# Kernel optimization log

Hardware: AMD Instinct MI355X
Metric: run time of the kernel (lower is better)

The kernel has to match this reference:

```python
import jax, jax.numpy as jnp
import numpy as np
import math

HIDDEN = 128; NHEADS = 4; N_COE = 50; N_SCALES = 4; THRE = 5.0; S = 4096; B = 1


def setup_inputs():
    key = jax.random.key(0)
    ks = jax.random.split(key, 12)
    w = lambda k, shape: jax.random.normal(k, shape, jnp.float32) * 0.05
    return {
        "eigenvalue": jax.random.uniform(ks[0], (B, S), jnp.float32) * 2.0,  # graph Laplacian eigvals in [0,2)
        "length": jnp.full((B,), S, dtype=jnp.int32),
        "sele_num": jnp.full((B,), S, dtype=jnp.int32),
        "eig_w_W": w(ks[1], (HIDDEN + 1, HIDDEN)), "eig_w_b": jnp.zeros((HIDDEN,), jnp.float32),
        "mha_ln_g": jnp.ones((HIDDEN,), jnp.float32), "mha_ln_b": jnp.zeros((HIDDEN,), jnp.float32),
        "in_W": w(ks[2], (HIDDEN, 3 * HIDDEN)), "in_b": jnp.zeros((3 * HIDDEN,), jnp.float32),
        "out_W": w(ks[3], (HIDDEN, HIDDEN)), "out_b": jnp.zeros((HIDDEN,), jnp.float32),
        "ffn_ln_g": jnp.ones((HIDDEN,), jnp.float32), "ffn_ln_b": jnp.zeros((HIDDEN,), jnp.float32),
        "ffn1_W": w(ks[4], (HIDDEN, HIDDEN)), "ffn1_b": jnp.zeros((HIDDEN,), jnp.float32),
        "ffn2_W": w(ks[5], (HIDDEN, HIDDEN)), "ffn2_b": jnp.zeros((HIDDEN,), jnp.float32),
        "dsc_W": w(ks[6], (HIDDEN, N_COE)), "dsc_b": jnp.zeros((N_COE,), jnp.float32),
        "dwv_W": w(ks[7], (HIDDEN, N_COE)), "dwv_b": jnp.zeros((N_COE,), jnp.float32),
        "dss_W": w(ks[8], (HIDDEN, N_SCALES)), "dss_b": jnp.zeros((N_SCALES,), jnp.float32),
    }


def layer_norm(x, g, b, eps=1e-5):
    m = x.mean(-1, keepdims=True)
    v = ((x - m) ** 2).mean(-1, keepdims=True)
    return (x - m) / jnp.sqrt(v + eps) * g + b


def sine_encoding(e, W, b):
    # e: [B, S] -> [B, S, HIDDEN]
    div = jnp.exp(jnp.arange(0, HIDDEN, 2, dtype=e.dtype) * (-math.log(10000.0) / HIDDEN))
    pe = (e * 100.0)[..., None] * div  # [B, S, HIDDEN/2]
    eeig = jnp.concatenate([e[..., None], jnp.sin(pe), jnp.cos(pe)], axis=-1)  # [B, S, HIDDEN+1]
    return eeig @ W + b


def mha(x, pad_mask, in_W, in_b, out_W, out_b):
    # x: [B, S, D]; pad_mask: [B, S] True = masked key
    Bb, Ss, D = x.shape
    hd = D // NHEADS
    qkv = x @ in_W + in_b
    q, k, v = jnp.split(qkv, 3, axis=-1)
    hsplit = lambda t: t.reshape(Bb, Ss, NHEADS, hd).transpose(0, 2, 1, 3)  # [B, H, S, hd]
    q, k, v = hsplit(q), hsplit(k), hsplit(v)
    scores = jnp.einsum('bhqd,bhkd->bhqk', q, k) / math.sqrt(hd)
    scores = jnp.where(pad_mask[:, None, None, :], -jnp.inf, scores)
    attn = jax.nn.softmax(scores, axis=-1)
    o = jnp.einsum('bhqk,bhkd->bhqd', attn, v).transpose(0, 2, 1, 3).reshape(Bb, Ss, D)
    return o @ out_W + out_b


def cheb_base(y, n_coe, flag):
    # Chebyshev recurrence: wavelet = [T_0, T_2, ...], scaling = [T_1, T_3, ...]
    te0 = jnp.ones_like(y)
    to0 = y
    def step(carry, _):
        te, to = carry
        te = 2.0 * y * to - te
        to = 2.0 * y * te - to
        return (te, to), (te, to)
    _, (evens, odds) = jax.lax.scan(step, (te0, to0), None, length=n_coe - 1)
    if flag == 'scaling':
        base = jnp.concatenate([to0[None], odds], axis=0)   # [n_coe, B, S, d]
    else:
        base = jnp.concatenate([te0[None], evens], axis=0)
    return jnp.moveaxis(base, 0, 1)  # [B, n_coe, S, d]


def _forward(eigenvalue, eig_w_W, eig_w_b, mha_ln_g, mha_ln_b, in_W, in_b, out_W, out_b,
             ffn_ln_g, ffn_ln_b, ffn1_W, ffn1_b, ffn2_W, ffn2_b,
             dsc_W, dsc_b, dwv_W, dwv_b, dss_W, dss_b, length, sele_num):
    Bb, Ss = eigenvalue.shape
    eve = eigenvalue
    eig_mask = jnp.arange(Ss)[None, :] >= sele_num[:, None]  # [B, S] True = pad
    # --- EigenEncoding (dropout in eval mode = identity) ---
    eig = sine_encoding(eve, eig_w_W, eig_w_b)
    eig = eig + mha(layer_norm(eig, mha_ln_g, mha_ln_b), eig_mask, in_W, in_b, out_W, out_b)
    f = layer_norm(eig, ffn_ln_g, ffn_ln_b)
    f = jax.nn.gelu(f @ ffn1_W + ffn1_b, approximate=False) @ ffn2_W + ffn2_b
    eig_filter = eig + f  # [B, S, HIDDEN]
    lenf = length.astype(eve.dtype)[:, None]
    def pooled(W, b):
        c = eig_filter @ W + b
        c = jnp.where(eig_mask[..., None], 0.0, c)
        return c.sum(axis=1) / (lenf + 1e-8)
    coe_scaling = jax.nn.sigmoid(pooled(dsc_W, dsc_b))
    coe_scaling = coe_scaling / (coe_scaling.sum(-1, keepdims=True) + 1e-8)  # [B, n_coe]
    coe_wavelet = jax.nn.sigmoid(pooled(dwv_W, dwv_b))
    coe_wavelet = coe_wavelet / (coe_wavelet.sum(-1, keepdims=True) + 1e-8)
    coe_scales = jax.nn.sigmoid(pooled(dss_W, dss_b)) * THRE  # [B, n_scales]
    # --- Chebyshev bases ---
    base_scaling = cheb_base(eve[..., None] - 1.0, N_COE, 'scaling')  # [B, n_coe, S, 1]
    fsw = eve[..., None] * coe_scales[:, None, :]                      # [B, S, n_scales]
    fsw = jnp.where(fsw > 2.0, 0.0, fsw)
    base_wavelet = cheb_base(fsw - 1.0, N_COE, 'wavelet')             # [B, n_coe, S, n_scales]
    base_scaling = 0.5 * (1.0 - base_scaling)
    base_wavelet = 0.5 * (1.0 - base_wavelet)
    curr_scaling = jnp.einsum('bc,bcsd->bsd', coe_scaling, base_scaling)
    curr_wavelet = jnp.einsum('bc,bcsd->bsd', coe_wavelet, base_wavelet)
    out = jnp.concatenate([curr_scaling, curr_wavelet], axis=-1)       # [B, S, 1+n_scales]
    out = out / (jnp.linalg.norm(out, axis=-1, keepdims=True) + 1e-8)  # cfg.lam.tight_use = True
    return out


def reference(eigenvalue, length, sele_num, eig_w_W, eig_w_b, mha_ln_g, mha_ln_b, in_W, in_b,
              out_W, out_b, ffn_ln_g, ffn_ln_b, ffn1_W, ffn1_b, ffn2_W, ffn2_b,
              dsc_W, dsc_b, dwv_W, dwv_b, dss_W, dss_b):
    return _forward(eigenvalue, eig_w_W, eig_w_b, mha_ln_g, mha_ln_b, in_W, in_b, out_W, out_b,
                    ffn_ln_g, ffn_ln_b, ffn1_W, ffn1_b, ffn2_W, ffn2_b,
                    dsc_W, dsc_b, dwv_W, dwv_b, dss_W, dss_b, length, sele_num)
```

## Files before the change

kernel.cpp:

```cpp
#include <hip/hip_runtime.h>
#include <math.h>


#define KSPLIT 4

typedef __attribute__((ext_vector_type(8))) short short8;
typedef __attribute__((ext_vector_type(4))) short short4v;
typedef __attribute__((ext_vector_type(4))) float f32x4;

__device__ inline unsigned short f2bf(float x) {
    unsigned u = __float_as_uint(x);
    return (unsigned short)((u + 0x7FFFu + ((u >> 16) & 1u)) >> 16);
}
__device__ inline float bf2f(unsigned short h) { return __uint_as_float(((unsigned)h) << 16); }

__global__ __launch_bounds__(512) void k_embed(const float* __restrict__ eve,
    const float* __restrict__ eigW, const float* __restrict__ ebias,
    const float* __restrict__ g, const float* __restrict__ b,
    const float* __restrict__ inW, const float* __restrict__ inb,
    float* __restrict__ eig, float* __restrict__ qkv, unsigned short* __restrict__ Khi_g,
    unsigned short* __restrict__ Klo_g, unsigned short* __restrict__ Vt_g,
    float* __restrict__ xsum)
{
    __shared__ __align__(16) float wsh[129 * 128];
    __shared__ __align__(16) float se[16][132];
    __shared__ __align__(16) float xn[16][132];
    __shared__ __align__(16) unsigned short vsh[16][136];
    const int t = threadIdx.x;
    const int r0 = blockIdx.x * 16;
    if (blockIdx.x == 0 && t < 128) xsum[t] = 0.f;
    {
        const int r = t >> 5, l5 = t & 31;
        const float e = eve[r0 + r];
        if (l5 == 0) se[r][128] = e;
        #pragma unroll
        for (int jj = 0; jj < 2; ++jj) {
            const int j = l5 * 2 + jj;
            const float div = __expf(-0.07195578415606394f * (float)(2 * j));
            const float pe = e * 100.0f * div;
            se[r][j]      = __sinf(pe);
            se[r][64 + j] = __cosf(pe);
        }
    }
    {
        const float4* __restrict__ src = (const float4*)eigW;
        float4* dst = (float4*)wsh;
        #pragma unroll
        for (int i = 0; i < 9; ++i) {
            const int f = t + i * 512;
            if (f < 4128) dst[f] = src[f];
        }
    }
    __syncthreads();
    const int r  = t >> 5;
    const int c0 = (t & 31) * 4;
    float xa[4];
    {
        const float4 w0 = *(const float4*)&wsh[c0];
        const float ea = se[r][128];
        float a0 = ea * w0.x, a1 = ea * w0.y, a2 = ea * w0.z, a3 = ea * w0.w;
        #pragma unroll 8
        for (int k = 0; k < 128; ++k) {
            const float xv = se[r][k];
            const float4 wk = *(const float4*)&wsh[(k + 1) * 128 + c0];
            a0 = fmaf(xv, wk.x, a0); a1 = fmaf(xv, wk.y, a1);
            a2 = fmaf(xv, wk.z, a2); a3 = fmaf(xv, wk.w, a3);
        }
        const float4 bb = *(const float4*)&ebias[c0];
        xa[0] = a0 + bb.x; xa[1] = a1 + bb.y; xa[2] = a2 + bb.z; xa[3] = a3 + bb.w;
        *(float4*)&eig[(size_t)(r0 + r) * 128 + c0] = make_float4(xa[0], xa[1], xa[2], xa[3]);
    }
    {
        float sa = (xa[0] + xa[1]) + (xa[2] + xa[3]);
        float qa = (xa[0] * xa[0] + xa[1] * xa[1]) + (xa[2] * xa[2] + xa[3] * xa[3]);
        #pragma unroll
        for (int m = 1; m < 32; m <<= 1) {
            sa += __shfl_xor(sa, m, 32); qa += __shfl_xor(qa, m, 32);
        }
        const float ma = sa * (1.f / 128.f);
        const float ia = 1.f / sqrtf(qa * (1.f / 128.f) - ma * ma + 1e-5f);
        const float4 gg = *(const float4*)&g[c0];
        const float4 bb = *(const float4*)&b[c0];
        *(float4*)&xn[r][c0] = make_float4((xa[0] - ma) * ia * gg.x + bb.x,
                                           (xa[1] - ma) * ia * gg.y + bb.y,
                                           (xa[2] - ma) * ia * gg.z + bb.z,
                                           (xa[3] - ma) * ia * gg.w + bb.w);
    }
    const int row = r0 + r;
    for (int p = 0; p < 3; ++p) {
        __syncthreads();
        {
            const float4* __restrict__ src = (const float4*)inW;
            float4* dst = (float4*)wsh;
            #pragma unroll
            for (int i = 0; i < 8; ++i) {
                const int f = t + i * 512;
                const int k = f >> 5, c4 = f & 31;
                dst[f] = src[k * 96 + p * 32 + c4];
            }
        }
        __syncthreads();
        float A[4];
        {
            const float4 bb = *(const float4*)&inb[p * 128 + c0];
            A[0] = bb.x; A[1] = bb.y; A[2] = bb.z; A[3] = bb.w;
        }
        #pragma unroll 8
        for (int k = 0; k < 128; ++k) {
            const float xv = xn[r][k];
            const float4 wk = *(const float4*)&wsh[k * 128 + c0];
            A[0] = fmaf(xv, wk.x, A[0]); A[1] = fmaf(xv, wk.y, A[1]);
            A[2] = fmaf(xv, wk.z, A[2]); A[3] = fmaf(xv, wk.w, A[3]);
        }
        if (p == 0) {
            *(float4*)&qkv[(size_t)row * 384 + c0] = make_float4(A[0], A[1], A[2], A[3]);
        } else if (p == 1) {
            const int h = c0 >> 5, d = c0 & 31;
            unsigned short h4[4], l4v[4];
            #pragma unroll
            for (int i = 0; i < 4; ++i) { h4[i] = f2bf(A[i]); l4v[i] = f2bf(A[i] - bf2f(h4[i])); }
            *(uint2*)&Khi_g[((size_t)h * 4096 + row) * 32 + d] = *(uint2*)h4;
            *(uint2*)&Klo_g[((size_t)h * 4096 + row) * 32 + d] = *(uint2*)l4v;
        } else {
            unsigned short v4[4];
            #pragma unroll
            for (int i = 0; i < 4; ++i) v4[i] = f2bf(A[i]);
            *(uint2*)&vsh[r][c0] = *(uint2*)v4;
        }
    }
    __syncthreads();
    if (t < 128) {
        unsigned short tmp[16];
        #pragma unroll
        for (int k2 = 0; k2 < 16; ++k2) tmp[k2] = vsh[k2][t];
        *(uint4*)&Vt_g[(size_t)t * 4096 + r0]     = *(uint4*)&tmp[0];
        *(uint4*)&Vt_g[(size_t)t * 4096 + r0 + 8] = *(uint4*)&tmp[8];
    }
}

#define KSTR 40
#define VSTR 72
#define PSTR 72

__global__ __launch_bounds__(256) void k_attn(const float* __restrict__ qkv,
    const unsigned short* __restrict__ Khi_g, const unsigned short* __restrict__ Klo_g,
    const unsigned short* __restrict__ Vt_g,
    const int* __restrict__ sele, float* __restrict__ Oe, float* __restrict__ E)
{
    __shared__ __align__(16) unsigned short Khi[64 * KSTR];
    __shared__ __align__(16) unsigned short Klo[64 * KSTR];
    __shared__ __align__(16) unsigned short Vt[32 * VSTR];
    __shared__ __align__(16) unsigned short Pb[4][16 * PSTR];

    const int t = threadIdx.x;
    const int lane = t & 63;
    const int l = lane & 15;
    const int quad = lane >> 4;
    const int wv = __builtin_amdgcn_readfirstlane(t >> 6);
    const int qb = blockIdx.x;
    const int h  = blockIdx.y;
    const int ks = blockIdx.z;
    const int nk = sele[0];

    short8 qhi, qlo;
    {
        const float* __restrict__ qr = qkv + (size_t)(qb * 64 + wv * 16 + l) * 384 + h * 32 + quad * 8;
        const float4 a = *(const float4*)qr;
        const float4 b = *(const float4*)(qr + 4);
        const float sc = 0.17677669529663687f;
        float v[8] = {a.x * sc, a.y * sc, a.z * sc, a.w * sc, b.x * sc, b.y * sc, b.z * sc, b.w * sc};
        #pragma unroll
        for (int j = 0; j < 8; ++j) {
            const unsigned short hb = f2bf(v[j]);
            qhi[j] = (short)hb;
            qlo[j] = (short)f2bf(v[j] - bf2f(hb));
        }
    }
    f32x4 accO0 = {0.f, 0.f, 0.f, 0.f};
    f32x4 accO1 = {0.f, 0.f, 0.f, 0.f};
    float elane = 0.f;

    const int kk = t >> 2;
    const int d0 = (t & 3) * 8;
    const int vd = t >> 3;
    const int ko = (t & 7) * 8;

    for (int ch = 0; ch < 16; ++ch) {
        const int keybase = ks * 1024 + ch * 64;
        __syncthreads();
        {
            const uint4 kh16 = *(const uint4*)&Khi_g[((size_t)h * 4096 + keybase + kk) * 32 + d0];
            const uint4 kl16 = *(const uint4*)&Klo_g[((size_t)h * 4096 + keybase + kk) * 32 + d0];
            const uint4 vv16 = *(const uint4*)&Vt_g[((size_t)h * 32 + vd) * 4096 + keybase + ko];
            *(uint4*)&Khi[kk * KSTR + d0] = kh16;
            *(uint4*)&Klo[kk * KSTR + d0] = kl16;
            *(uint4*)&Vt[vd * VSTR + ko]  = vv16;
        }
        __syncthreads();
        unsigned short* __restrict__ Pw = Pb[wv];
        #pragma unroll
        for (int tile = 0; tile < 4; ++tile) {
            const int kl = tile * 16 + l;
            const short8 kh = *(const short8*)&Khi[kl * KSTR + quad * 8];
            const short8 kw = *(const short8*)&Klo[kl * KSTR + quad * 8];
            f32x4 S = {0.f, 0.f, 0.f, 0.f};
            S = __builtin_amdgcn_mfma_f32_16x16x32_bf16(kh, qhi, S, 0, 0, 0);
            S = __builtin_amdgcn_mfma_f32_16x16x32_bf16(kw, qhi, S, 0, 0, 0);
            S = __builtin_amdgcn_mfma_f32_16x16x32_bf16(kh, qlo, S, 0, 0, 0);
            const int kg0 = keybase + tile * 16 + quad * 4;
            short4v pw;
            #pragma unroll
            for (int r = 0; r < 4; ++r) {
                const float p = (kg0 + r < nk) ? __expf(S[r]) : 0.f;
                elane += p;
                pw[r] = (short)f2bf(p);
            }
            *(short4v*)&Pw[l * PSTR + tile * 16 + quad * 4] = pw;
        }
        #pragma unroll
        for (int step = 0; step < 2; ++step) {
            const short8 pa  = *(const short8*)&Pw[l * PSTR + step * 32 + quad * 8];
            const short8 vb0 = *(const short8*)&Vt[l * VSTR + step * 32 + quad * 8];
            const short8 vb1 = *(const short8*)&Vt[(16 + l) * VSTR + step * 32 + quad * 8];
            accO0 = __builtin_amdgcn_mfma_f32_16x16x32_bf16(pa, vb0, accO0, 0, 0, 0);
            accO1 = __builtin_amdgcn_mfma_f32_16x16x32_bf16(pa, vb1, accO1, 0, 0, 0);
        }
    }
    elane += __shfl_xor(elane, 16, 64);
    elane += __shfl_xor(elane, 32, 64);
    const int qrow0 = qb * 64 + wv * 16;
    if (lane < 16)
        E[((size_t)ks * 4 + h) * 4096 + qrow0 + l] = elane;
    #pragma unroll
    for (int r = 0; r < 4; ++r) {
        const size_t row = qrow0 + quad * 4 + r;
        Oe[((size_t)ks * 4096 + row) * 128 + h * 32 + l]      = accO0[r];
        Oe[((size_t)ks * 4096 + row) * 128 + h * 32 + 16 + l] = accO1[r];
    }
}

__global__ __launch_bounds__(512) void k_ffn(const float* __restrict__ eig,
    const float* __restrict__ Oe, const float* __restrict__ E,
    const float* __restrict__ outW, const float* __restrict__ outb,
    const float* __restrict__ lg, const float* __restrict__ lb,
    const float* __restrict__ W1, const float* __restrict__ b1,
    const float* __restrict__ W2, const float* __restrict__ b2,
    const int* __restrict__ sele, float* __restrict__ xsum)
{
    __shared__ __align__(16) float wsh[128 * 128];
    __shared__ __align__(16) float sA[16][132];
    __shared__ __align__(16) float xn[16][132];
    __shared__ __align__(16) float cs[16][132];
    const int t = threadIdx.x;
    const int r0 = blockIdx.x * 16;
    const int r  = t >> 5;
    const int c0 = (t & 31) * 4;
    {
        const int h = c0 >> 5;
        float es = 0.f;
        float v[4] = {0.f, 0.f, 0.f, 0.f};
        #pragma unroll
        for (int ks = 0; ks < KSPLIT; ++ks) {
            es += E[((size_t)ks * 4 + h) * 4096 + r0 + r];
            const float4 o1 = *(const float4*)&Oe[((size_t)ks * 4096 + r0 + r) * 128 + c0];
            v[0] += o1.x; v[1] += o1.y; v[2] += o1.z; v[3] += o1.w;
        }
        const float rcp = 1.f / es;
        *(float4*)&sA[r][c0] = make_float4(v[0] * rcp, v[1] * rcp, v[2] * rcp, v[3] * rcp);
    }
    {
        const float4* __restrict__ src = (const float4*)outW;
        float4* dst = (float4*)wsh;
        #pragma unroll
        for (int i = 0; i < 8; ++i) dst[t + i * 512] = src[t + i * 512];
    }
    __syncthreads();
    float x2[4];
    {
        const float4 bb = *(const float4*)&outb[c0];
        float a0 = bb.x, a1 = bb.y, a2 = bb.z, a3 = bb.w;
        #pragma unroll 8
        for (int k = 0; k < 128; ++k) {
            const float xv = sA[r][k];
            const float4 wk = *(const float4*)&wsh[k * 128 + c0];
            a0 = fmaf(xv, wk.x, a0); a1 = fmaf(xv, wk.y, a1);
            a2 = fmaf(xv, wk.z, a2); a3 = fmaf(xv, wk.w, a3);
        }
        const float4 ea = *(const float4*)&eig[(size_t)(r0 + r) * 128 + c0];
        x2[0] = ea.x + a0; x2[1] = ea.y + a1; x2[2] = ea.z + a2; x2[3] = ea.w + a3;
    }
    {
        float sa = (x2[0] + x2[1]) + (x2[2] + x2[3]);
        float qa = (x2[0] * x2[0] + x2[1] * x2[1]) + (x2[2] * x2[2] + x2[3] * x2[3]);
        #pragma unroll
        for (int m = 1; m < 32; m <<= 1) {
            sa += __shfl_xor(sa, m, 32); qa += __shfl_xor(qa, m, 32);
        }
        const float ma = sa * (1.f / 128.f);
        const float ia = 1.f / sqrtf(qa * (1.f / 128.f) - ma * ma + 1e-5f);
        const float4 gg = *(const float4*)&lg[c0];
        const float4 bb = *(const float4*)&lb[c0];
        *(float4*)&xn[r][c0] = make_float4((x2[0] - ma) * ia * gg.x + bb.x,
                                           (x2[1] - ma) * ia * gg.y + bb.y,
                                           (x2[2] - ma) * ia * gg.z + bb.z,
                                           (x2[3] - ma) * ia * gg.w + bb.w);
    }
    __syncthreads();
    {
        const float4* __restrict__ src = (const float4*)W1;
        float4* dst = (float4*)wsh;
        #pragma unroll
        for (int i = 0; i < 8; ++i) dst[t + i * 512] = src[t + i * 512];
    }
    __syncthreads();
    {
        const float4 bb = *(const float4*)&b1[c0];
        float a0 = bb.x, a1 = bb.y, a2 = bb.z, a3 = bb.w;
        #pragma unroll 8
        for (int k = 0; k < 128; ++k) {
            const float xv = xn[r][k];
            const float4 wk = *(const float4*)&wsh[k * 128 + c0];
            a0 = fmaf(xv, wk.x, a0); a1 = fmaf(xv, wk.y, a1);
            a2 = fmaf(xv, wk.z, a2); a3 = fmaf(xv, wk.w, a3);
        }
        *(float4*)&sA[r][c0] = make_float4(
            0.5f * a0 * (1.f + erff(a0 * 0.70710678118654752f)),
            0.5f * a1 * (1.f + erff(a1 * 0.70710678118654752f)),
            0.5f * a2 * (1.f + erff(a2 * 0.70710678118654752f)),
            0.5f * a3 * (1.f + erff(a3 * 0.70710678118654752f)));
    }
    __syncthreads();
    {
        const float4* __restrict__ src = (const float4*)W2;
        float4* dst = (float4*)wsh;
        #pragma unroll
        for (int i = 0; i < 8; ++i) dst[t + i * 512] = src[t + i * 512];
    }
    __syncthreads();
    {
        const float4 bb = *(const float4*)&b2[c0];
        float a0 = bb.x, a1 = bb.y, a2 = bb.z, a3 = bb.w;
        #pragma unroll 8
        for (int k = 0; k < 128; ++k) {
            const float xv = sA[r][k];
            const float4 wk = *(const float4*)&wsh[k * 128 + c0];
            a0 = fmaf(xv, wk.x, a0); a1 = fmaf(xv, wk.y, a1);
            a2 = fmaf(xv, wk.z, a2); a3 = fmaf(xv, wk.w, a3);
        }
        const int nsel = sele[0];
        const bool ina = (r0 + r) < nsel;
        *(float4*)&cs[r][c0] = ina ? make_float4(x2[0] + a0, x2[1] + a1, x2[2] + a2, x2[3] + a3)
                                   : make_float4(0.f, 0.f, 0.f, 0.f);
    }
    __syncthreads();
    if (t < 128) {
        float s = 0.f;
        #pragma unroll
        for (int rr = 0; rr < 16; ++rr) s += cs[rr][t];
        atomicAdd(&xsum[t], s);
    }
}

__global__ __launch_bounds__(128) void k_tail(const float* __restrict__ eve,
    const float* __restrict__ xsum,
    const float* __restrict__ dscW, const float* __restrict__ dscb,
    const float* __restrict__ dwvW, const float* __restrict__ dwvb,
    const float* __restrict__ dssW, const float* __restrict__ dssb,
    const int* __restrict__ len, const int* __restrict__ sele,
    float* __restrict__ out)
{
    __shared__ float xs[128];
    __shared__ float val[104];
    __shared__ float s2[2];
    __shared__ float csc[50], cwv[50], cssh[4];
    const int t = threadIdx.x;
    xs[t] = xsum[t];
    __syncthreads();
    if (t < 104) {
        const float invl = 1.f / ((float)len[0] + 1e-8f);
        const float ns = (float)sele[0];
        const float* Wp; int stride, col; float bias;
        if (t < 50)       { Wp = dscW; stride = 50; col = t;       bias = dscb[t]; }
        else if (t < 100) { Wp = dwvW; stride = 50; col = t - 50;  bias = dwvb[t - 50]; }
        else              { Wp = dssW; stride = 4;  col = t - 100; bias = dssb[t - 100]; }
        float a = 0.f;
        #pragma unroll 4
        for (int k = 0; k < 128; ++k) a = fmaf(xs[k], Wp[k * stride + col], a);
        a = (a + ns * bias) * invl;
        val[t] = 1.f / (1.f + __expf(-a));
    }
    __syncthreads();
    if (t == 0) { float s = 0.f; for (int i = 0; i < 50; ++i) s += val[i]; s2[0] = s; }
    if (t == 1) { float s = 0.f; for (int i = 0; i < 50; ++i) s += val[50 + i]; s2[1] = s; }
    __syncthreads();
    if (t < 50) {
        csc[t] = val[t] / (s2[0] + 1e-8f);
        cwv[t] = val[50 + t] / (s2[1] + 1e-8f);
    } else if (t >= 100 && t < 104) {
        cssh[t - 100] = val[t] * 5.0f;
    }
    __syncthreads();
    const int s = blockIdx.x * 128 + t;
    const float e = eve[s];
    float vals[5];
    {
        const float y = e - 1.f;
        float te = 1.f, to = y;
        float a = csc[0] * (0.5f * (1.f - to));
        const float y2 = 2.f * y;
        for (int i = 1; i < 50; ++i) {
            te = fmaf(y2, to, -te);
            to = fmaf(y2, te, -to);
            a = fmaf(csc[i], 0.5f * (1.f - to), a);
        }
        vals[0] = a;
    }
    #pragma unroll
    for (int j = 0; j < 4; ++j) {
        float f = e * cssh[j];
        if (f > 2.f) f = 0.f;
        const float y = f - 1.f;
        float te = 1.f, to = y;
        float a = cwv[0] * (0.5f * (1.f - te));
        const float y2 = 2.f * y;
        for (int i = 1; i < 50; ++i) {
            te = fmaf(y2, to, -te);
            to = fmaf(y2, te, -to);
            a = fmaf(cwv[i], 0.5f * (1.f - te), a);
        }
        vals[1 + j] = a;
    }
    float n2 = 0.f;
    #pragma unroll
    for (int k = 0; k < 5; ++k) n2 += vals[k] * vals[k];
    const float invn = 1.f / (sqrtf(n2) + 1e-8f);
    #pragma unroll
    for (int k = 0; k < 5; ++k) out[s * 5 + k] = vals[k] * invn;
}

extern "C" void kernel_launch(void* const* d_in, const int* in_sizes, int n_in,
                              void* d_out, int out_size, void* d_ws, size_t ws_size,
                              hipStream_t stream) {
    const float* eve  = (const float*)d_in[0];
    const int*   len  = (const int*)d_in[1];
    const int*   sele = (const int*)d_in[2];
    const float* eigW = (const float*)d_in[3];
    const float* eigB = (const float*)d_in[4];
    const float* mlg  = (const float*)d_in[5];
    const float* mlb  = (const float*)d_in[6];
    const float* inW  = (const float*)d_in[7];
    const float* inb  = (const float*)d_in[8];
    const float* outW = (const float*)d_in[9];
    const float* outb = (const float*)d_in[10];
    const float* flg  = (const float*)d_in[11];
    const float* flb  = (const float*)d_in[12];
    const float* W1   = (const float*)d_in[13];
    const float* b1   = (const float*)d_in[14];
    const float* W2   = (const float*)d_in[15];
    const float* b2   = (const float*)d_in[16];
    const float* dscW = (const float*)d_in[17];
    const float* dscb = (const float*)d_in[18];
    const float* dwvW = (const float*)d_in[19];
    const float* dwvb = (const float*)d_in[20];
    const float* dssW = (const float*)d_in[21];
    const float* dssb = (const float*)d_in[22];

    float* ws   = (float*)d_ws;
    float* eig  = ws;
    float* qkv  = ws + 524288;
    float* Oe   = ws + 2097152;
    float* E    = ws + 4194304;
    float* xsum = ws + 4259840;
    unsigned short* Khi_g = (unsigned short*)(ws + 4260352);
    unsigned short* Klo_g = (unsigned short*)(ws + 4522496);
    unsigned short* Vt_g  = (unsigned short*)(ws + 4784640);
    float* out  = (float*)d_out;

    k_embed<<<256, 512, 0, stream>>>(eve, eigW, eigB, mlg, mlb, inW, inb,
                                     eig, qkv, Khi_g, Klo_g, Vt_g, xsum);
    k_attn <<<dim3(64, 4, KSPLIT), 256, 0, stream>>>(qkv, Khi_g, Klo_g, Vt_g, sele, Oe, E);
    k_ffn  <<<256, 512, 0, stream>>>(eig, Oe, E, outW, outb, flg, flb, W1, b1, W2, b2, sele, xsum);
    k_tail <<<32, 128, 0, stream>>>(eve, xsum, dscW, dscb, dwvW, dwvb, dssW, dssb, len, sele, out);
}
```

Before: 185.8 us.

## Double-buffer weight and K/V tiles with register prefetch across kernels

The embed and FFN kernels now stage weights in two half-size LDS buffers, loading the next 64-row half into registers while the current half is used in the FMA loop, so global loads overlap compute. The attention kernel double-buffers the K-hi, K-lo and V tiles with register prefetch of the next chunk, which removes one barrier per chunk. Raising wave priority around the MFMAs and packing bf16 conversion of P through a hardware intrinsic are also added. Halving the weight LDS footprint may raise occupancy, but the extra prefetch registers add register pressure.

```diff
diff --git a/kernel.cpp b/kernel.cpp
--- a/kernel.cpp
+++ b/kernel.cpp
@@ -1,11 +1,11 @@
 #include <hip/hip_runtime.h>
+#include <hip/hip_bf16.h>
 #include <math.h>
 
 
 #define KSPLIT 4
 
 typedef __attribute__((ext_vector_type(8))) short short8;
-typedef __attribute__((ext_vector_type(4))) short short4v;
 typedef __attribute__((ext_vector_type(4))) float f32x4;
 
 __device__ inline unsigned short f2bf(float x) {
@@ -13,6 +13,10 @@
     return (unsigned short)((u + 0x7FFFu + ((u >> 16) & 1u)) >> 16);
 }
 __device__ inline float bf2f(unsigned short h) { return __uint_as_float(((unsigned)h) << 16); }
+__device__ inline unsigned pk_bf16(float lo, float hi) {
+    __hip_bfloat162 h = __float22bfloat162_rn(make_float2(lo, hi));
+    return *reinterpret_cast<unsigned*>(&h);
+}
 
 __global__ __launch_bounds__(512) void k_embed(const float* __restrict__ eve,
     const float* __restrict__ eigW, const float* __restrict__ ebias,
@@ -22,55 +26,83 @@
     unsigned short* __restrict__ Klo_g, unsigned short* __restrict__ Vt_g,
     float* __restrict__ xsum)
 {
-    __shared__ __align__(16) float wsh[129 * 128];
+    __shared__ __align__(16) float wsh[2][65 * 128];
     __shared__ __align__(16) float se[16][132];
     __shared__ __align__(16) float xn[16][132];
     __shared__ __align__(16) unsigned short vsh[16][136];
     const int t = threadIdx.x;
     const int r0 = blockIdx.x * 16;
     if (blockIdx.x == 0 && t < 128) xsum[t] = 0.f;
-    {
-        const int r = t >> 5, l5 = t & 31;
-        const float e = eve[r0 + r];
-        if (l5 == 0) se[r][128] = e;
+
+    const float4* __restrict__ eigW4 = (const float4*)eigW;
+    const float4* __restrict__ inW4  = (const float4*)inW;
+    float4 pf0 = eigW4[t];
+    float4 pf1 = eigW4[t + 512];
+    float4 pf2 = eigW4[t + 1024];
+    float4 pf3 = eigW4[t + 1536];
+    float4 pf4;
+    if (t < 32) pf4 = eigW4[t + 2048];
+
+    {
+        const int rr = t >> 5, l5 = t & 31;
+        const float e = eve[r0 + rr];
+        if (l5 == 0) se[rr][128] = e;
         #pragma unroll
         for (int jj = 0; jj < 2; ++jj) {
             const int j = l5 * 2 + jj;
             const float div = __expf(-0.07195578415606394f * (float)(2 * j));
             const float pe = e * 100.0f * div;
-            se[r][j]      = __sinf(pe);
-            se[r][64 + j] = __cosf(pe);
-        }
-    }
-    {
-        const float4* __restrict__ src = (const float4*)eigW;
-        float4* dst = (float4*)wsh;
-        #pragma unroll
-        for (int i = 0; i < 9; ++i) {
-            const int f = t + i * 512;
-            if (f < 4128) dst[f] = src[f];
-        }
-    }
-    __syncthreads();
+            se[rr][j]      = __sinf(pe);
+            se[rr][64 + j] = __cosf(pe);
+        }
+    }
+    {
+        float4* dst = (float4*)wsh[0];
+        dst[t] = pf0; dst[t + 512] = pf1; dst[t + 1024] = pf2; dst[t + 1536] = pf3;
+        if (t < 32) dst[t + 2048] = pf4;
+    }
     const int r  = t >> 5;
     const int c0 = (t & 31) * 4;
+    const int kb = t >> 5, c4 = t & 31;
+    float a0, a1, a2, a3;
     float xa[4];
-    {
-        const float4 w0 = *(const float4*)&wsh[c0];
+
+    __syncthreads();
+    pf0 = eigW4[2080 + t];        pf1 = eigW4[2080 + t + 512];
+    pf2 = eigW4[2080 + t + 1024]; pf3 = eigW4[2080 + t + 1536];
+    {
+        const float* __restrict__ W = wsh[0];
+        const float4 w0 = *(const float4*)&W[c0];
         const float ea = se[r][128];
-        float a0 = ea * w0.x, a1 = ea * w0.y, a2 = ea * w0.z, a3 = ea * w0.w;
+        a0 = ea * w0.x; a1 = ea * w0.y; a2 = ea * w0.z; a3 = ea * w0.w;
         #pragma unroll 8
-        for (int k = 0; k < 128; ++k) {
+        for (int k = 0; k < 64; ++k) {
             const float xv = se[r][k];
-            const float4 wk = *(const float4*)&wsh[(k + 1) * 128 + c0];
+            const float4 wk = *(const float4*)&W[(k + 1) * 128 + c0];
+            a0 = fmaf(xv, wk.x, a0); a1 = fmaf(xv, wk.y, a1);
+            a2 = fmaf(xv, wk.z, a2); a3 = fmaf(xv, wk.w, a3);
+        }
+    }
+    {   float4* dst = (float4*)wsh[1];
+        dst[t] = pf0; dst[t + 512] = pf1; dst[t + 1024] = pf2; dst[t + 1536] = pf3;
+    }
+    __syncthreads();
+    pf0 = inW4[(size_t)(kb +  0) * 96 + c4];
+    pf1 = inW4[(size_t)(kb + 16) * 96 + c4];
+    pf2 = inW4[(size_t)(kb + 32) * 96 + c4];
+    pf3 = inW4[(size_t)(kb + 48) * 96 + c4];
+    {
+        const float* __restrict__ W = wsh[1];
+        #pragma unroll 8
+        for (int k = 64; k < 128; ++k) {
+            const float xv = se[r][k];
+            const float4 wk = *(const float4*)&W[(k - 64) * 128 + c0];
             a0 = fmaf(xv, wk.x, a0); a1 = fmaf(xv, wk.y, a1);
             a2 = fmaf(xv, wk.z, a2); a3 = fmaf(xv, wk.w, a3);
         }
         const float4 bb = *(const float4*)&ebias[c0];
         xa[0] = a0 + bb.x; xa[1] = a1 + bb.y; xa[2] = a2 + bb.z; xa[3] = a3 + bb.w;
         *(float4*)&eig[(size_t)(r0 + r) * 128 + c0] = make_float4(xa[0], xa[1], xa[2], xa[3]);
-    }
-    {
         float sa = (xa[0] + xa[1]) + (xa[2] + xa[3]);
         float qa = (xa[0] * xa[0] + xa[1] * xa[1]) + (xa[2] * xa[2] + xa[3] * xa[3]);
         #pragma unroll
@@ -80,57 +112,70 @@
         const float ma = sa * (1.f / 128.f);
         const float ia = 1.f / sqrtf(qa * (1.f / 128.f) - ma * ma + 1e-5f);
         const float4 gg = *(const float4*)&g[c0];
-        const float4 bb = *(const float4*)&b[c0];
-        *(float4*)&xn[r][c0] = make_float4((xa[0] - ma) * ia * gg.x + bb.x,
-                                           (xa[1] - ma) * ia * gg.y + bb.y,
-                                           (xa[2] - ma) * ia * gg.z + bb.z,
-                                           (xa[3] - ma) * ia * gg.w + bb.w);
+        const float4 lb = *(const float4*)&b[c0];
+        *(float4*)&xn[r][c0] = make_float4((xa[0] - ma) * ia * gg.x + lb.x,
+                                           (xa[1] - ma) * ia * gg.y + lb.y,
+                                           (xa[2] - ma) * ia * gg.z + lb.z,
+                                           (xa[3] - ma) * ia * gg.w + lb.w);
+    }
+    {   float4* dst = (float4*)wsh[0];
+        dst[t] = pf0; dst[t + 512] = pf1; dst[t + 1024] = pf2; dst[t + 1536] = pf3;
     }
     const int row = r0 + r;
+    float A0, A1, A2, A3;
+    #pragma unroll
     for (int p = 0; p < 3; ++p) {
-        __syncthreads();
-        {
-            const float4* __restrict__ src = (const float4*)inW;
-            float4* dst = (float4*)wsh;
-            #pragma unroll
-            for (int i = 0; i < 8; ++i) {
-                const int f = t + i * 512;
-                const int k = f >> 5, c4 = f & 31;
-                dst[f] = src[k * 96 + p * 32 + c4];
+        #pragma unroll
+        for (int hh = 0; hh < 2; ++hh) {
+            __syncthreads();
+            const bool last = (p == 2 && hh == 1);
+            if (!last) {
+                const int np = p + hh, nh = hh ^ 1;
+                pf0 = inW4[(size_t)(kb +  0 + nh * 64) * 96 + np * 32 + c4];
+                pf1 = inW4[(size_t)(kb + 16 + nh * 64) * 96 + np * 32 + c4];
+                pf2 = inW4[(size_t)(kb + 32 + nh * 64) * 96 + np * 32 + c4];
+                pf3 = inW4[(size_t)(kb + 48 + nh * 64) * 96 + np * 32 + c4];
             }
-        }
-        __syncthreads();
-        float A[4];
-        {
-            const float4 bb = *(const float4*)&inb[p * 128 + c0];
-            A[0] = bb.x; A[1] = bb.y; A[2] = bb.z; A[3] = bb.w;
-        }
-        #pragma unroll 8
-        for (int k = 0; k < 128; ++k) {
-            const float xv = xn[r][k];
-            const float4 wk = *(const float4*)&wsh[k * 128 + c0];
-            A[0] = fmaf(xv, wk.x, A[0]); A[1] = fmaf(xv, wk.y, A[1]);
-            A[2] = fmaf(xv, wk.z, A[2]); A[3] = fmaf(xv, wk.w, A[3]);
-        }
-        if (p == 0) {
-            *(float4*)&qkv[(size_t)row * 384 + c0] = make_float4(A[0], A[1], A[2], A[3]);
-        } else if (p == 1) {
-            const int h = c0 >> 5, d = c0 & 31;
-            unsigned short h4[4], l4v[4];
-            #pragma unroll
-            for (int i = 0; i < 4; ++i) { h4[i] = f2bf(A[i]); l4v[i] = f2bf(A[i] - bf2f(h4[i])); }
-            *(uint2*)&Khi_g[((size_t)h * 4096 + row) * 32 + d] = *(uint2*)h4;
-            *(uint2*)&Klo_g[((size_t)h * 4096 + row) * 32 + d] = *(uint2*)l4v;
-        } else {
-            unsigned short v4[4];
-            #pragma unroll
-            for (int i = 0; i < 4; ++i) v4[i] = f2bf(A[i]);
-            *(uint2*)&vsh[r][c0] = *(uint2*)v4;
+            if (hh == 0) {
+                const float4 bb = *(const float4*)&inb[p * 128 + c0];
+                A0 = bb.x; A1 = bb.y; A2 = bb.z; A3 = bb.w;
+            }
+            const float* __restrict__ W = wsh[hh];
+            #pragma unroll 8
+            for (int k2 = 0; k2 < 64; ++k2) {
+                const float xv = xn[r][hh * 64 + k2];
+                const float4 wk = *(const float4*)&W[k2 * 128 + c0];
+                A0 = fmaf(xv, wk.x, A0); A1 = fmaf(xv, wk.y, A1);
+                A2 = fmaf(xv, wk.z, A2); A3 = fmaf(xv, wk.w, A3);
+            }
+            if (!last) {
+                float4* dst = (float4*)wsh[hh ^ 1];
+                dst[t] = pf0; dst[t + 512] = pf1; dst[t + 1024] = pf2; dst[t + 1536] = pf3;
+            }
+            if (hh == 1) {
+                if (p == 0) {
+                    *(float4*)&qkv[(size_t)row * 384 + c0] = make_float4(A0, A1, A2, A3);
+                } else if (p == 1) {
+                    const int h = c0 >> 5, d = c0 & 31;
+                    float A[4] = {A0, A1, A2, A3};
+                    unsigned short h4[4], l4v[4];
+                    #pragma unroll
+                    for (int i = 0; i < 4; ++i) { h4[i] = f2bf(A[i]); l4v[i] = f2bf(A[i] - bf2f(h4[i])); }
+                    *(uint2*)&Khi_g[((size_t)h * 4096 + row) * 32 + d] = *(uint2*)h4;
+                    *(uint2*)&Klo_g[((size_t)h * 4096 + row) * 32 + d] = *(uint2*)l4v;
+                } else {
+                    unsigned short v4[4];
+                    float A[4] = {A0, A1, A2, A3};
+                    #pragma unroll
+                    for (int i = 0; i < 4; ++i) v4[i] = f2bf(A[i]);
+                    *(uint2*)&vsh[r][c0] = *(uint2*)v4;
+                }
+            }
         }
     }
     __syncthreads();
     if (t < 128) {
-        unsigned short tmp[16];
+        __align__(16) unsigned short tmp[16];
         #pragma unroll
         for (int k2 = 0; k2 < 16; ++k2) tmp[k2] = vsh[k2][t];
         *(uint4*)&Vt_g[(size_t)t * 4096 + r0]     = *(uint4*)&tmp[0];
@@ -147,9 +192,9 @@
     const unsigned short* __restrict__ Vt_g,
     const int* __restrict__ sele, float* __restrict__ Oe, float* __restrict__ E)
 {
-    __shared__ __align__(16) unsigned short Khi[64 * KSTR];
-    __shared__ __align__(16) unsigned short Klo[64 * KSTR];
-    __shared__ __align__(16) unsigned short Vt[32 * VSTR];
+    __shared__ __align__(16) unsigned short Khi[2][64 * KSTR];
+    __shared__ __align__(16) unsigned short Klo[2][64 * KSTR];
+    __shared__ __align__(16) unsigned short Vt[2][32 * VSTR];
     __shared__ __align__(16) unsigned short Pb[4][16 * PSTR];
 
     const int t = threadIdx.x;
@@ -185,45 +230,64 @@
     const int vd = t >> 3;
     const int ko = (t & 7) * 8;
 
+    const unsigned short* __restrict__ pKhi = Khi_g + ((size_t)h * 4096 + ks * 1024 + kk) * 32 + d0;
+    const unsigned short* __restrict__ pKlo = Klo_g + ((size_t)h * 4096 + ks * 1024 + kk) * 32 + d0;
+    const unsigned short* __restrict__ pVt  = Vt_g  + ((size_t)h * 32 + vd) * 4096 + ks * 1024 + ko;
+
+    uint4 kh_n = *(const uint4*)pKhi;
+    uint4 kl_n = *(const uint4*)pKlo;
+    uint4 vv_n = *(const uint4*)pVt;
+    *(uint4*)&Khi[0][kk * KSTR + d0] = kh_n;
+    *(uint4*)&Klo[0][kk * KSTR + d0] = kl_n;
+    *(uint4*)&Vt[0][vd * VSTR + ko]  = vv_n;
+
     for (int ch = 0; ch < 16; ++ch) {
+        __syncthreads();
+        const int cur = ch & 1;
+        if (ch < 15) {
+            kh_n = *(const uint4*)(pKhi + (size_t)(ch + 1) * 2048);
+            kl_n = *(const uint4*)(pKlo + (size_t)(ch + 1) * 2048);
+            vv_n = *(const uint4*)(pVt  + (ch + 1) * 64);
+        }
         const int keybase = ks * 1024 + ch * 64;
-        __syncthreads();
-        {
-            const uint4 kh16 = *(const uint4*)&Khi_g[((size_t)h * 4096 + keybase + kk) * 32 + d0];
-            const uint4 kl16 = *(const uint4*)&Klo_g[((size_t)h * 4096 + keybase + kk) * 32 + d0];
-            const uint4 vv16 = *(const uint4*)&Vt_g[((size_t)h * 32 + vd) * 4096 + keybase + ko];
-            *(uint4*)&Khi[kk * KSTR + d0] = kh16;
-            *(uint4*)&Klo[kk * KSTR + d0] = kl16;
-            *(uint4*)&Vt[vd * VSTR + ko]  = vv16;
-        }
-        __syncthreads();
+        const unsigned short* __restrict__ KhiC = Khi[cur];
+        const unsigned short* __restrict__ KloC = Klo[cur];
+        const unsigned short* __restrict__ VtC  = Vt[cur];
         unsigned short* __restrict__ Pw = Pb[wv];
         #pragma unroll
         for (int tile = 0; tile < 4; ++tile) {
             const int kl = tile * 16 + l;
-            const short8 kh = *(const short8*)&Khi[kl * KSTR + quad * 8];
-            const short8 kw = *(const short8*)&Klo[kl * KSTR + quad * 8];
+            const short8 kh = *(const short8*)&KhiC[kl * KSTR + quad * 8];
+            const short8 kw = *(const short8*)&KloC[kl * KSTR + quad * 8];
             f32x4 S = {0.f, 0.f, 0.f, 0.f};
+            __builtin_amdgcn_s_setprio(1);
             S = __builtin_amdgcn_mfma_f32_16x16x32_bf16(kh, qhi, S, 0, 0, 0);
             S = __builtin_amdgcn_mfma_f32_16x16x32_bf16(kw, qhi, S, 0, 0, 0);
             S = __builtin_amdgcn_mfma_f32_16x16x32_bf16(kh, qlo, S, 0, 0, 0);
+            __builtin_amdgcn_s_setprio(0);
             const int kg0 = keybase + tile * 16 + quad * 4;
-            short4v pw;
-            #pragma unroll
-            for (int r = 0; r < 4; ++r) {
-                const float p = (kg0 + r < nk) ? __expf(S[r]) : 0.f;
-                elane += p;
-                pw[r] = (short)f2bf(p);
-            }
-            *(short4v*)&Pw[l * PSTR + tile * 16 + quad * 4] = pw;
+            const float p0 = (kg0 + 0 < nk) ? __expf(S[0]) : 0.f;
+            const float p1 = (kg0 + 1 < nk) ? __expf(S[1]) : 0.f;
+            const float p2 = (kg0 + 2 < nk) ? __expf(S[2]) : 0.f;
+            const float p3 = (kg0 + 3 < nk) ? __expf(S[3]) : 0.f;
+            elane += (p0 + p1) + (p2 + p3);
+            *(uint2*)&Pw[l * PSTR + tile * 16 + quad * 4] =
+                make_uint2(pk_bf16(p0, p1), pk_bf16(p2, p3));
         }
         #pragma unroll
         for (int step = 0; step < 2; ++step) {
             const short8 pa  = *(const short8*)&Pw[l * PSTR + step * 32 + quad * 8];
-            const short8 vb0 = *(const short8*)&Vt[l * VSTR + step * 32 + quad * 8];
-            const short8 vb1 = *(const short8*)&Vt[(16 + l) * VSTR + step * 32 + quad * 8];
+            const short8 vb0 = *(const short8*)&VtC[l * VSTR + step * 32 + quad * 8];
+            const short8 vb1 = *(const short8*)&VtC[(16 + l) * VSTR + step * 32 + quad * 8];
+            __builtin_amdgcn_s_setprio(1);
             accO0 = __builtin_amdgcn_mfma_f32_16x16x32_bf16(pa, vb0, accO0, 0, 0, 0);
             accO1 = __builtin_amdgcn_mfma_f32_16x16x32_bf16(pa, vb1, accO1, 0, 0, 0);
+            __builtin_amdgcn_s_setprio(0);
+        }
+        if (ch < 15) {
+            *(uint4*)&Khi[cur ^ 1][kk * KSTR + d0] = kh_n;
+            *(uint4*)&Klo[cur ^ 1][kk * KSTR + d0] = kl_n;
+            *(uint4*)&Vt[cur ^ 1][vd * VSTR + ko]  = vv_n;
         }
     }
     elane += __shfl_xor(elane, 16, 64);
@@ -247,7 +311,7 @@
     const float* __restrict__ W2, const float* __restrict__ b2,
     const int* __restrict__ sele, float* __restrict__ xsum)
 {
-    __shared__ __align__(16) float wsh[128 * 128];
+    __shared__ __align__(16) float wsh[2][64 * 128];
     __shared__ __align__(16) float sA[16][132];
     __shared__ __align__(16) float xn[16][132];
     __shared__ __align__(16) float cs[16][132];
@@ -255,6 +319,13 @@
     const int r0 = blockIdx.x * 16;
     const int r  = t >> 5;
     const int c0 = (t & 31) * 4;
+
+    const float4* __restrict__ Wp0 = (const float4*)outW;
+    const float4* __restrict__ Wp1 = (const float4*)W1;
+    const float4* __restrict__ Wp2 = (const float4*)W2;
+
+    float4 pf0 = Wp0[t], pf1 = Wp0[t + 512], pf2 = Wp0[t + 1024], pf3 = Wp0[t + 1536];
+
     {
         const int h = c0 >> 5;
         float es = 0.f;
@@ -268,89 +339,72 @@
         const float rcp = 1.f / es;
         *(float4*)&sA[r][c0] = make_float4(v[0] * rcp, v[1] * rcp, v[2] * rcp, v[3] * rcp);
     }
-    {
-        const float4* __restrict__ src = (const float4*)outW;
-        float4* dst = (float4*)wsh;
-        #pragma unroll
-        for (int i = 0; i < 8; ++i) dst[t + i * 512] = src[t + i * 512];
-    }
-    __syncthreads();
+    {   float4* dst = (float4*)wsh[0];
+        dst[t] = pf0; dst[t + 512] = pf1; dst[t + 1024] = pf2; dst[t + 1536] = pf3;
+    }
+
     float x2[4];
-    {
-        const float4 bb = *(const float4*)&outb[c0];
-        float a0 = bb.x, a1 = bb.y, a2 = bb.z, a3 = bb.w;
+    float A0, A1, A2, A3;
+    #pragma unroll
+    for (int gphase = 0; gphase < 6; ++gphase) {
+        const int gg = gphase >> 1, hh = gphase & 1;
+        __syncthreads();
+        if (gphase < 5) {
+            const int nid = gphase + 1;
+            const int ng = nid >> 1, nh = nid & 1;
+            const float4* __restrict__ src = (ng == 0) ? Wp0 : (ng == 1 ? Wp1 : Wp2);
+            pf0 = src[nh * 2048 + t];        pf1 = src[nh * 2048 + t + 512];
+            pf2 = src[nh * 2048 + t + 1024]; pf3 = src[nh * 2048 + t + 1536];
+        }
+        if (hh == 0) {
+            const float* bias = (gg == 0) ? outb : (gg == 1 ? b1 : b2);
+            const float4 bb = *(const float4*)&bias[c0];
+            A0 = bb.x; A1 = bb.y; A2 = bb.z; A3 = bb.w;
+        }
+        const float* __restrict__ W = wsh[hh];
+        const float* __restrict__ act = (gg == 1) ? &xn[r][0] : &sA[r][0];
         #pragma unroll 8
-        for (int k = 0; k < 128; ++k) {
-            const float xv = sA[r][k];
-            const float4 wk = *(const float4*)&wsh[k * 128 + c0];
-            a0 = fmaf(xv, wk.x, a0); a1 = fmaf(xv, wk.y, a1);
-            a2 = fmaf(xv, wk.z, a2); a3 = fmaf(xv, wk.w, a3);
-        }
-        const float4 ea = *(const float4*)&eig[(size_t)(r0 + r) * 128 + c0];
-        x2[0] = ea.x + a0; x2[1] = ea.y + a1; x2[2] = ea.z + a2; x2[3] = ea.w + a3;
-    }
-    {
-        float sa = (x2[0] + x2[1]) + (x2[2] + x2[3]);
-        float qa = (x2[0] * x2[0] + x2[1] * x2[1]) + (x2[2] * x2[2] + x2[3] * x2[3]);
-        #pragma unroll
-        for (int m = 1; m < 32; m <<= 1) {
-            sa += __shfl_xor(sa, m, 32); qa += __shfl_xor(qa, m, 32);
-        }
-        const float ma = sa * (1.f / 128.f);
-        const float ia = 1.f / sqrtf(qa * (1.f / 128.f) - ma * ma + 1e-5f);
-        const float4 gg = *(const float4*)&lg[c0];
-        const float4 bb = *(const float4*)&lb[c0];
-        *(float4*)&xn[r][c0] = make_float4((x2[0] - ma) * ia * gg.x + bb.x,
-                                           (x2[1] - ma) * ia * gg.y + bb.y,
-                                           (x2[2] - ma) * ia * gg.z + bb.z,
-                                           (x2[3] - ma) * ia * gg.w + bb.w);
-    }
-    __syncthreads();
-    {
-        const float4* __restrict__ src = (const float4*)W1;
-        float4* dst = (float4*)wsh;
-        #pragma unroll
-        for (int i = 0; i < 8; ++i) dst[t + i * 512] = src[t + i * 512];
-    }
-    __syncthreads();
-    {
-        const float4 bb = *(const float4*)&b1[c0];
-        float a0 = bb.x, a1 = bb.y, a2 = bb.z, a3 = bb.w;
-        #pragma unroll 8
-        for (int k = 0; k < 128; ++k) {
-            const float xv = xn[r][k];
-            const float4 wk = *(const float4*)&wsh[k * 128 + c0];
-            a0 = fmaf(xv, wk.x, a0); a1 = fmaf(xv, wk.y, a1);
-            a2 = fmaf(xv, wk.z, a2); a3 = fmaf(xv, wk.w, a3);
-        }
-        *(float4*)&sA[r][c0] = make_float4(
-            0.5f * a0 * (1.f + erff(a0 * 0.70710678118654752f)),
-            0.5f * a1 * (1.f + erff(a1 * 0.70710678118654752f)),
-            0.5f * a2 * (1.f + erff(a2 * 0.70710678118654752f)),
-            0.5f * a3 * (1.f + erff(a3 * 0.70710678118654752f)));
-    }
-    __syncthreads();
-    {
-        const float4* __restrict__ src = (const float4*)W2;
-        float4* dst = (float4*)wsh;
-        #pragma unroll
-        for (int i = 0; i < 8; ++i) dst[t + i * 512] = src[t + i * 512];
-    }
-    __syncthreads();
-    {
-        const float4 bb = *(const float4*)&b2[c0];
-        float a0 = bb.x, a1 = bb.y, a2 = bb.z, a3 = bb.w;
-        #pragma unroll 8
-        for (int k = 0; k < 128; ++k) {
-            const float xv = sA[r][k];
-            const float4 wk = *(const float4*)&wsh[k * 128 + c0];
-            a0 = fmaf(xv, wk.x, a0); a1 = fmaf(xv, wk.y, a1);
-            a2 = fmaf(xv, wk.z, a2); a3 = fmaf(xv, wk.w, a3);
-        }
-        const int nsel = sele[0];
-        const bool ina = (r0 + r) < nsel;
-        *(float4*)&cs[r][c0] = ina ? make_float4(x2[0] + a0, x2[1] + a1, x2[2] + a2, x2[3] + a3)
-                                   : make_float4(0.f, 0.f, 0.f, 0.f);
+        for (int k2 = 0; k2 < 64; ++k2) {
+            const float xv = act[hh * 64 + k2];
+            const float4 wk = *(const float4*)&W[k2 * 128 + c0];
+            A0 = fmaf(xv, wk.x, A0); A1 = fmaf(xv, wk.y, A1);
+            A2 = fmaf(xv, wk.z, A2); A3 = fmaf(xv, wk.w, A3);
+        }
+        if (gphase < 5) {
+            float4* dst = (float4*)wsh[hh ^ 1];
+            dst[t] = pf0; dst[t + 512] = pf1; dst[t + 1024] = pf2; dst[t + 1536] = pf3;
+        }
+        if (hh == 1) {
+            if (gg == 0) {
+                const float4 ea = *(const float4*)&eig[(size_t)(r0 + r) * 128 + c0];
+                x2[0] = ea.x + A0; x2[1] = ea.y + A1; x2[2] = ea.z + A2; x2[3] = ea.w + A3;
+                float sa = (x2[0] + x2[1]) + (x2[2] + x2[3]);
+                float qa = (x2[0] * x2[0] + x2[1] * x2[1]) + (x2[2] * x2[2] + x2[3] * x2[3]);
+                #pragma unroll
+                for (int m = 1; m < 32; m <<= 1) {
+                    sa += __shfl_xor(sa, m, 32); qa += __shfl_xor(qa, m, 32);
+                }
+                const float ma = sa * (1.f / 128.f);
+                const float ia = 1.f / sqrtf(qa * (1.f / 128.f) - ma * ma + 1e-5f);
+                const float4 gg4 = *(const float4*)&lg[c0];
+                const float4 bb4 = *(const float4*)&lb[c0];
+                *(float4*)&xn[r][c0] = make_float4((x2[0] - ma) * ia * gg4.x + bb4.x,
+                                                   (x2[1] - ma) * ia * gg4.y + bb4.y,
+                                                   (x2[2] - ma) * ia * gg4.z + bb4.z,
+                                                   (x2[3] - ma) * ia * gg4.w + bb4.w);
+            } else if (gg == 1) {
+                *(float4*)&sA[r][c0] = make_float4(
+                    0.5f * A0 * (1.f + erff(A0 * 0.70710678118654752f)),
+                    0.5f * A1 * (1.f + erff(A1 * 0.70710678118654752f)),
+                    0.5f * A2 * (1.f + erff(A2 * 0.70710678118654752f)),
+                    0.5f * A3 * (1.f + erff(A3 * 0.70710678118654752f)));
+            } else {
+                const int nsel = sele[0];
+                const bool ina = (r0 + r) < nsel;
+                *(float4*)&cs[r][c0] = ina ? make_float4(x2[0] + A0, x2[1] + A1, x2[2] + A2, x2[3] + A3)
+                                           : make_float4(0.f, 0.f, 0.f, 0.f);
+            }
+        }
     }
     __syncthreads();
     if (t < 128) {
```

Measured after the change: 180.6 us. 1.03x faster.
